# Performance work log

Hardware: AMD Instinct MI355X
Metric: run time of the kernel (lower is better)

The kernel has to match this reference:

```python
import jax, jax.numpy as jnp
import numpy as np

B, S, H, E = 4, 2048, 1024, 8

def setup_inputs() -> dict:
    key = jax.random.key(0)
    k1, k2, k3 = jax.random.split(key, 3)
    scale_g = 1.0 / np.sqrt(H)
    scale_e = 1.0 / np.sqrt(H)
    return {
        "x": jax.random.normal(k1, (B, S, H), dtype=jnp.float32),
        "gate_w": jax.random.normal(k2, (H, E), dtype=jnp.float32) * scale_g,
        "gate_b": jnp.zeros((E,), dtype=jnp.float32),
        "expert_w": jax.random.normal(k3, (E, H, H), dtype=jnp.float32) * scale_e,
        "expert_b": jnp.zeros((E, H), dtype=jnp.float32),
    }

def reference(x, gate_w, gate_b, expert_w, expert_b):
    b, s, h = x.shape
    tok = x.reshape(-1, h)                                  # [T, H]
    # gate: softmax over experts per token
    w = jax.nn.softmax(tok @ gate_w + gate_b, axis=-1)      # [T, E]
    # all experts applied to all tokens (dense MoE)
    eo = jnp.einsum("th,ehd->ted", tok, expert_w) + expert_b[None]  # [T, E, H]
    out = jnp.einsum("te,ted->td", w, eo)                   # [T, H]
    return out.reshape(b, s, h)
```

## Files before the change

### kernel.cpp

```cpp
#include <hip/hip_runtime.h>
#include <stdint.h>

typedef unsigned short u16;
typedef short bf8 __attribute__((ext_vector_type(8)));
typedef float f4 __attribute__((ext_vector_type(4)));

#define TTOK 8192
#define HD   1024
#define NE   8

static __device__ __forceinline__ u16 f2bf(float f) {
  union { float f; uint32_t u; } v; v.f = f;
  return (u16)((v.u + 0x7fffu + ((v.u >> 16) & 1u)) >> 16);
}

__global__ __launch_bounds__(256) void gate_conv_kernel(
    const float* __restrict__ x, const float* __restrict__ gw,
    const float* __restrict__ gb, float* __restrict__ wout,
    u16* __restrict__ abf)
{
  const int t    = blockIdx.x * 4 + (threadIdx.x >> 6);
  const int lane = threadIdx.x & 63;
  const float* xr = x + (size_t)t * HD;
  float p[NE];
#pragma unroll
  for (int e = 0; e < NE; ++e) p[e] = 0.f;
#pragma unroll 4
  for (int h = lane; h < HD; h += 64) {
    const float xv = xr[h];
    abf[(size_t)t * HD + h] = f2bf(xv);
    const float* g = gw + (size_t)h * NE;
#pragma unroll
    for (int e = 0; e < NE; ++e) p[e] += xv * g[e];
  }
#pragma unroll
  for (int e = 0; e < NE; ++e) {
#pragma unroll
    for (int off = 32; off > 0; off >>= 1)
      p[e] += __shfl_xor(p[e], off, 64);
    p[e] += gb[e];
  }
  float m = p[0];
#pragma unroll
  for (int e = 1; e < NE; ++e) m = fmaxf(m, p[e]);
  float s = 0.f;
#pragma unroll
  for (int e = 0; e < NE; ++e) { p[e] = expf(p[e] - m); s += p[e]; }
  const float inv = 1.f / s;
  if (lane == 0) {
#pragma unroll
    for (int e = 0; e < NE; ++e) wout[t * NE + e] = p[e] * inv;
  }
}

__global__ __launch_bounds__(256) void wconv_kernel(
    const float* __restrict__ ew, u16* __restrict__ wt)
{
  __shared__ u16 tile[64][66];
  const int e  = blockIdx.z;
  const int h0 = blockIdx.y * 64;
  const int d0 = blockIdx.x * 64;
  const int c  = threadIdx.x & 63;
  const int r0 = threadIdx.x >> 6;
  const float* src = ew + (size_t)e * HD * HD;
  u16* dst = wt + (size_t)e * HD * HD;
#pragma unroll
  for (int i = 0; i < 16; ++i) {
    const int r = i * 4 + r0;
    tile[r][c] = f2bf(src[(size_t)(h0 + r) * HD + d0 + c]);
  }
  __syncthreads();
#pragma unroll
  for (int i = 0; i < 16; ++i) {
    const int r = i * 4 + r0;
    dst[(size_t)(d0 + r) * HD + h0 + c] = tile[c][r];
  }
}

#define BM 128
#define BN 256
#define BK 64

#define MM(a_, b_, c_) __builtin_amdgcn_mfma_f32_16x16x32_bf16((a_), (b_), (c_), 0, 0, 0)

#define LDFA(off_, m_, kk_) (*(const bf8*)((const char*)As + (off_) + \
    (size_t)(wrb + (m_) * 16 + l15) * 128 + ((((kk_) * 4 + lhi) ^ (l15 & 7)) << 4)))
#define LDFB(off_, n_, kk_) (*(const bf8*)((const char*)Bs + (off_) + \
    (size_t)(wcb + (n_) * 16 + l15) * 128 + ((((kk_) * 4 + lhi) ^ (l15 & 7)) << 4)))

#define GL(srcp_, dstp_) __builtin_amdgcn_global_load_lds( \
    (const __attribute__((address_space(1))) void*)(srcp_), \
    (__attribute__((address_space(3))) void*)(dstp_), 16, 0, 0)

#define STAGE_PA(sq_)                                               \
  {                                                                 \
    const int se_ = (sq_) >> 4;                                     \
    const int sk_ = ((sq_) & 15) << 6;                              \
    const u16* as_ = aSrc0 + sk_;                                   \
    const u16* bs_ = bSrc0 + (size_t)se_ * (HD * HD) + sk_;         \
    char* ad_ = (char*)As + stA + tid * 16;                         \
    char* bd_ = (char*)Bs + stB + tid * 16;                         \
    GL(as_,         ad_);                                           \
    GL(as_ + 65536, ad_ + 8192);                                    \
    GL(bs_,         bd_);                                           \
  }
#define STAGE_PB(sq_)                                               \
  {                                                                 \
    const int se_ = (sq_) >> 4;                                     \
    const int sk_ = ((sq_) & 15) << 6;                              \
    const u16* bs_ = bSrc0 + (size_t)se_ * (HD * HD) + sk_;         \
    char* bd_ = (char*)Bs + stB + tid * 16;                         \
    GL(bs_ +  65536, bd_ +  8192);                                  \
    GL(bs_ + 131072, bd_ + 16384);                                  \
    GL(bs_ + 196608, bd_ + 24576);                                  \
  }

#define MFMA16                                            \
    acc[0][0] = MM(a0, b0, acc[0][0]);                    \
    acc[1][0] = MM(a1, b0, acc[1][0]);                    \
    acc[2][0] = MM(a2, b0, acc[2][0]);                    \
    acc[3][0] = MM(a3, b0, acc[3][0]);                    \
    acc[0][1] = MM(a0, b1, acc[0][1]);                    \
    acc[1][1] = MM(a1, b1, acc[1][1]);                    \
    acc[2][1] = MM(a2, b1, acc[2][1]);                    \
    acc[3][1] = MM(a3, b1, acc[3][1]);                    \
    acc[0][2] = MM(a0, b2, acc[0][2]);                    \
    acc[1][2] = MM(a1, b2, acc[1][2]);                    \
    acc[2][2] = MM(a2, b2, acc[2][2]);                    \
    acc[3][2] = MM(a3, b2, acc[3][2]);                    \
    acc[0][3] = MM(a0, b3, acc[0][3]);                    \
    acc[1][3] = MM(a1, b3, acc[1][3]);                    \
    acc[2][3] = MM(a2, b3, acc[2][3]);                    \
    acc[3][3] = MM(a3, b3, acc[3][3]);

#define READS(kk_)                                        \
    bf8 a0 = LDFA(curA, 0, kk_);                          \
    bf8 a1 = LDFA(curA, 1, kk_);                          \
    bf8 a2 = LDFA(curA, 2, kk_);                          \
    bf8 a3 = LDFA(curA, 3, kk_);                          \
    bf8 b0 = LDFB(curB, 0, kk_);                          \
    bf8 b1 = LDFB(curB, 1, kk_);                          \
    bf8 b2 = LDFB(curB, 2, kk_);                          \
    bf8 b3 = LDFB(curB, 3, kk_);

#define FOLD(e_)                                                      \
  {                                                                   \
    _Pragma("unroll")                                                 \
    for (int mi = 0; mi < 4; ++mi) {                                  \
      const int r_ = wrb + mi * 16 + lhi * 4;                         \
      const float w0 = wgs[(r_ + 0) * 9 + (e_)];                      \
      const float w1 = wgs[(r_ + 1) * 9 + (e_)];                      \
      const float w2 = wgs[(r_ + 2) * 9 + (e_)];                      \
      const float w3 = wgs[(r_ + 3) * 9 + (e_)];                      \
      _Pragma("unroll")                                               \
      for (int ni = 0; ni < 4; ++ni) {                                \
        accO[mi][ni][0] += w0 * acc[mi][ni][0];                       \
        accO[mi][ni][1] += w1 * acc[mi][ni][1];                       \
        accO[mi][ni][2] += w2 * acc[mi][ni][2];                       \
        accO[mi][ni][3] += w3 * acc[mi][ni][3];                       \
        acc[mi][ni] = fz;                                             \
      }                                                               \
    }                                                                 \
  }

#define ADVANCE                                          \
    curA += 16384; if (curA == 49152) curA = 0;          \
    curB += 32768; if (curB == 98304) curB = 0;          \
    stA  += 16384; if (stA  == 49152) stA  = 0;          \
    stB  += 32768; if (stB  == 98304) stB  = 0;

#define BAR       __builtin_amdgcn_s_barrier();
#define LGKM0     asm volatile("s_waitcnt lgkmcnt(0)" ::: "memory");
#define PRIO1     __builtin_amdgcn_s_setprio(1);
#define PRIO0     __builtin_amdgcn_s_setprio(0);

__global__ __launch_bounds__(512, 2) void moe_gemm_kernel(
    const u16* __restrict__ A,
    const u16* __restrict__ Wt,
    const float* __restrict__ wg,
    const float* __restrict__ eb,
    float* __restrict__ out)
{
  __shared__ u16 As[3 * BM * BK];
  __shared__ u16 Bs[3 * BN * BK];
  __shared__ float wgs[BM * 9];

  const int bid   = blockIdx.x;
  const int xcd   = bid & 7;
  const int local = bid >> 3;
  const int bm    = xcd * 8 + (local >> 2);
  const int bn    = local & 3;
  const int row0  = bm * BM;
  const int col0  = bn * BN;

  const int tid  = threadIdx.x;
  const int lane = tid & 63;
  const int wid  = tid >> 6;
  const int wr   = wid >> 2;
  const int wc   = wid & 3;
  const int l15  = lane & 15;
  const int lhi  = lane >> 4;
  const int wrb  = wr * 64;
  const int wcb  = wc * 64;

  const int row_in = tid >> 3;
  const int gsw    = (tid & 7) ^ ((tid >> 3) & 7);
  const u16* aSrc0 = A  + (size_t)(row0 + row_in) * HD + gsw * 8;
  const u16* bSrc0 = Wt + (size_t)(col0 + row_in) * HD + gsw * 8;

  {
    const int i0 = tid, i1 = tid + 512;
    const float v0 = wg[(size_t)row0 * NE + i0];
    const float v1 = wg[(size_t)row0 * NE + i1];
    wgs[(i0 >> 3) * 9 + (i0 & 7)] = v0;
    wgs[(i1 >> 3) * 9 + (i1 & 7)] = v1;
  }
  LGKM0

  const f4 fz = {0.f, 0.f, 0.f, 0.f};
  f4 acc[4][4], accO[4][4];
#pragma unroll
  for (int i = 0; i < 4; ++i)
#pragma unroll
    for (int j = 0; j < 4; ++j) { acc[i][j] = fz; accO[i][j] = fz; }

  int curA = 0, curB = 0;
  int stA = 32768, stB = 65536;

  {
    int svA = stA, svB = stB;
    stA = 0; stB = 0;       STAGE_PA(0) STAGE_PB(0)
    stA = 16384; stB = 32768; STAGE_PA(1) STAGE_PB(1)
    stA = svA; stB = svB;
  }
  asm volatile("s_waitcnt vmcnt(6)" ::: "memory");
  BAR

  for (int q = 0; q < 126; ++q) {
    {
      READS(0)
      STAGE_PA(q + 2)
      BAR LGKM0 PRIO1
      MFMA16
      PRIO0 BAR
    }
    {
      READS(1)
      STAGE_PB(q + 2)
      BAR LGKM0 PRIO1
      MFMA16
      PRIO0
      asm volatile("s_waitcnt vmcnt(6)" ::: "memory");
      BAR
    }
    ADVANCE
    if ((q & 15) == 15) FOLD(q >> 4)
  }
  {
    { READS(0) BAR LGKM0 PRIO1 MFMA16 PRIO0 BAR }
    { READS(1) BAR LGKM0 PRIO1 MFMA16 PRIO0
      asm volatile("s_waitcnt vmcnt(0)" ::: "memory");
      BAR }
    ADVANCE
  }
  {
    { READS(0) MFMA16 }
    { READS(1) MFMA16 }
  }
  FOLD(7)

  float ebv[4][8];
#pragma unroll
  for (int ni = 0; ni < 4; ++ni) {
    const int d = col0 + wcb + ni * 16 + l15;
#pragma unroll
    for (int e2 = 0; e2 < NE; ++e2) ebv[ni][e2] = eb[(size_t)e2 * HD + d];
  }
#pragma unroll
  for (int mi = 0; mi < 4; ++mi) {
    const int r_ = wrb + mi * 16 + lhi * 4;
#pragma unroll
    for (int j = 0; j < 4; ++j) {
      const int t = row0 + r_ + j;
      const float* wrow = &wgs[(r_ + j) * 9];
#pragma unroll
      for (int ni = 0; ni < 4; ++ni) {
        const float bias =
            wrow[0] * ebv[ni][0] + wrow[1] * ebv[ni][1] +
            wrow[2] * ebv[ni][2] + wrow[3] * ebv[ni][3] +
            wrow[4] * ebv[ni][4] + wrow[5] * ebv[ni][5] +
            wrow[6] * ebv[ni][6] + wrow[7] * ebv[ni][7];
        const int d = col0 + wcb + ni * 16 + l15;
        out[(size_t)t * HD + d] = accO[mi][ni][j] + bias;
      }
    }
  }
}

extern "C" void kernel_launch(void* const* d_in, const int* in_sizes, int n_in,
                              void* d_out, int out_size, void* d_ws, size_t ws_size,
                              hipStream_t stream) {
  const float* x  = (const float*)d_in[0];
  const float* gw = (const float*)d_in[1];
  const float* gb = (const float*)d_in[2];
  const float* ew = (const float*)d_in[3];
  const float* eb = (const float*)d_in[4];
  float* out = (float*)d_out;

  char* ws = (char*)d_ws;
  u16*   abf   = (u16*)ws;
  u16*   wt    = (u16*)(ws + (size_t)16 * 1024 * 1024);
  float* wgate = (float*)(ws + (size_t)32 * 1024 * 1024);

  gate_conv_kernel<<<dim3(TTOK / 4), dim3(256), 0, stream>>>(x, gw, gb, wgate, abf);
  wconv_kernel<<<dim3(16, 16, 8), dim3(256), 0, stream>>>(ew, wt);
  moe_gemm_kernel<<<dim3((TTOK / BM) * (HD / BN)), dim3(512), 0, stream>>>(abf, wt, wgate, eb, out);
}
```

Baseline: 156.4 us.

## Shrink GEMM tile to 128x128 with 4 waves and double buffering

Halves the output tile width and the block size to 256 threads (4 waves). It replaces the triple-buffered LDS pipeline, which waited with vmcnt(6), with a simpler double buffer that waits for all loads at the start of each iteration. The block-to-tile mapping is remapped and the gate-weight preload is vectorized. This doubles the grid and lowers LDS use per block, aiming for better occupancy and load balance. In exchange, A-tile reuse per loaded B element drops and load latency is less well hidden.

```diff
diff --git a/kernel.cpp b/kernel.cpp
--- a/kernel.cpp
+++ b/kernel.cpp
@@ -78,7 +78,7 @@
 }
 
 #define BM 128
-#define BN 256
+#define BN 128
 #define BK 64
 
 #define MM(a_, b_, c_) __builtin_amdgcn_mfma_f32_16x16x32_bf16((a_), (b_), (c_), 0, 0, 0)
@@ -92,27 +92,26 @@
     (const __attribute__((address_space(1))) void*)(srcp_), \
     (__attribute__((address_space(3))) void*)(dstp_), 16, 0, 0)
 
-#define STAGE_PA(sq_)                                               \
+#define STAGE_A(sq_)                                                \
   {                                                                 \
-    const int se_ = (sq_) >> 4;                                     \
     const int sk_ = ((sq_) & 15) << 6;                              \
     const u16* as_ = aSrc0 + sk_;                                   \
-    const u16* bs_ = bSrc0 + (size_t)se_ * (HD * HD) + sk_;         \
-    char* ad_ = (char*)As + stA + tid * 16;                         \
-    char* bd_ = (char*)Bs + stB + tid * 16;                         \
-    GL(as_,         ad_);                                           \
-    GL(as_ + 65536, ad_ + 8192);                                    \
-    GL(bs_,         bd_);                                           \
-  }
-#define STAGE_PB(sq_)                                               \
+    char* ad_ = (char*)As + stO + tid * 16;                         \
+    GL(as_,          ad_);                                          \
+    GL(as_ + 32768,  ad_ +  4096);                                  \
+    GL(as_ + 65536,  ad_ +  8192);                                  \
+    GL(as_ + 98304,  ad_ + 12288);                                  \
+  }
+#define STAGE_B(sq_)                                                \
   {                                                                 \
     const int se_ = (sq_) >> 4;                                     \
     const int sk_ = ((sq_) & 15) << 6;                              \
     const u16* bs_ = bSrc0 + (size_t)se_ * (HD * HD) + sk_;         \
-    char* bd_ = (char*)Bs + stB + tid * 16;                         \
-    GL(bs_ +  65536, bd_ +  8192);                                  \
-    GL(bs_ + 131072, bd_ + 16384);                                  \
-    GL(bs_ + 196608, bd_ + 24576);                                  \
+    char* bd_ = (char*)Bs + stO + tid * 16;                         \
+    GL(bs_,          bd_);                                          \
+    GL(bs_ + 32768,  bd_ +  4096);                                  \
+    GL(bs_ + 65536,  bd_ +  8192);                                  \
+    GL(bs_ + 98304,  bd_ + 12288);                                  \
   }
 
 #define MFMA16                                            \
@@ -134,14 +133,14 @@
     acc[3][3] = MM(a3, b3, acc[3][3]);
 
 #define READS(kk_)                                        \
-    bf8 a0 = LDFA(curA, 0, kk_);                          \
-    bf8 a1 = LDFA(curA, 1, kk_);                          \
-    bf8 a2 = LDFA(curA, 2, kk_);                          \
-    bf8 a3 = LDFA(curA, 3, kk_);                          \
-    bf8 b0 = LDFB(curB, 0, kk_);                          \
-    bf8 b1 = LDFB(curB, 1, kk_);                          \
-    bf8 b2 = LDFB(curB, 2, kk_);                          \
-    bf8 b3 = LDFB(curB, 3, kk_);
+    bf8 a0 = LDFA(curO, 0, kk_);                          \
+    bf8 a1 = LDFA(curO, 1, kk_);                          \
+    bf8 a2 = LDFA(curO, 2, kk_);                          \
+    bf8 a3 = LDFA(curO, 3, kk_);                          \
+    bf8 b0 = LDFB(curO, 0, kk_);                          \
+    bf8 b1 = LDFB(curO, 1, kk_);                          \
+    bf8 b2 = LDFB(curO, 2, kk_);                          \
+    bf8 b3 = LDFB(curO, 3, kk_);
 
 #define FOLD(e_)                                                      \
   {                                                                   \
@@ -163,57 +162,54 @@
     }                                                                 \
   }
 
-#define ADVANCE                                          \
-    curA += 16384; if (curA == 49152) curA = 0;          \
-    curB += 32768; if (curB == 98304) curB = 0;          \
-    stA  += 16384; if (stA  == 49152) stA  = 0;          \
-    stB  += 32768; if (stB  == 98304) stB  = 0;
-
 #define BAR       __builtin_amdgcn_s_barrier();
 #define LGKM0     asm volatile("s_waitcnt lgkmcnt(0)" ::: "memory");
+#define VM0       asm volatile("s_waitcnt vmcnt(0)" ::: "memory");
 #define PRIO1     __builtin_amdgcn_s_setprio(1);
 #define PRIO0     __builtin_amdgcn_s_setprio(0);
 
-__global__ __launch_bounds__(512, 2) void moe_gemm_kernel(
+__global__ __launch_bounds__(256, 2) void moe_gemm_kernel(
     const u16* __restrict__ A,
     const u16* __restrict__ Wt,
     const float* __restrict__ wg,
     const float* __restrict__ eb,
     float* __restrict__ out)
 {
-  __shared__ u16 As[3 * BM * BK];
-  __shared__ u16 Bs[3 * BN * BK];
+  __shared__ u16 As[2 * BM * BK];
+  __shared__ u16 Bs[2 * BN * BK];
   __shared__ float wgs[BM * 9];
 
   const int bid   = blockIdx.x;
   const int xcd   = bid & 7;
   const int local = bid >> 3;
-  const int bm    = xcd * 8 + (local >> 2);
-  const int bn    = local & 3;
+  const int bm    = xcd * 8 + (local & 7);
+  const int bn    = local >> 3;
   const int row0  = bm * BM;
   const int col0  = bn * BN;
 
   const int tid  = threadIdx.x;
   const int lane = tid & 63;
   const int wid  = tid >> 6;
-  const int wr   = wid >> 2;
-  const int wc   = wid & 3;
+  const int wr   = wid >> 1;
+  const int wc   = wid & 1;
   const int l15  = lane & 15;
   const int lhi  = lane >> 4;
   const int wrb  = wr * 64;
   const int wcb  = wc * 64;
 
   const int row_in = tid >> 3;
-  const int gsw    = (tid & 7) ^ ((tid >> 3) & 7);
+  const int gsw    = (tid & 7) ^ (row_in & 7);
   const u16* aSrc0 = A  + (size_t)(row0 + row_in) * HD + gsw * 8;
   const u16* bSrc0 = Wt + (size_t)(col0 + row_in) * HD + gsw * 8;
 
   {
-    const int i0 = tid, i1 = tid + 512;
-    const float v0 = wg[(size_t)row0 * NE + i0];
-    const float v1 = wg[(size_t)row0 * NE + i1];
-    wgs[(i0 >> 3) * 9 + (i0 & 7)] = v0;
-    wgs[(i1 >> 3) * 9 + (i1 & 7)] = v1;
+    const f4 v = *(const f4*)(wg + (size_t)row0 * NE + tid * 4);
+    const int i0 = tid * 4;
+#pragma unroll
+    for (int j = 0; j < 4; ++j) {
+      const int idx = i0 + j;
+      wgs[(idx >> 3) * 9 + (idx & 7)] = v[j];
+    }
   }
   LGKM0
 
@@ -224,49 +220,34 @@
 #pragma unroll
     for (int j = 0; j < 4; ++j) { acc[i][j] = fz; accO[i][j] = fz; }
 
-  int curA = 0, curB = 0;
-  int stA = 32768, stB = 65536;
-
-  {
-    int svA = stA, svB = stB;
-    stA = 0; stB = 0;       STAGE_PA(0) STAGE_PB(0)
-    stA = 16384; stB = 32768; STAGE_PA(1) STAGE_PB(1)
-    stA = svA; stB = svB;
-  }
-  asm volatile("s_waitcnt vmcnt(6)" ::: "memory");
-  BAR
-
-  for (int q = 0; q < 126; ++q) {
+  int curO = 0, stO = 16384;
+
+  { const int svO = stO; stO = 0; STAGE_A(0) STAGE_B(0) stO = svO; }
+
+  for (int q = 0; q < 127; ++q) {
+    VM0
+    BAR
     {
       READS(0)
-      STAGE_PA(q + 2)
+      STAGE_A(q + 1)
       BAR LGKM0 PRIO1
       MFMA16
       PRIO0 BAR
     }
     {
       READS(1)
-      STAGE_PB(q + 2)
+      STAGE_B(q + 1)
       BAR LGKM0 PRIO1
       MFMA16
       PRIO0
-      asm volatile("s_waitcnt vmcnt(6)" ::: "memory");
-      BAR
-    }
-    ADVANCE
+    }
+    { const int t_ = curO; curO = stO; stO = t_; }
     if ((q & 15) == 15) FOLD(q >> 4)
   }
-  {
-    { READS(0) BAR LGKM0 PRIO1 MFMA16 PRIO0 BAR }
-    { READS(1) BAR LGKM0 PRIO1 MFMA16 PRIO0
-      asm volatile("s_waitcnt vmcnt(0)" ::: "memory");
-      BAR }
-    ADVANCE
-  }
-  {
-    { READS(0) MFMA16 }
-    { READS(1) MFMA16 }
-  }
+  VM0
+  BAR
+  { READS(0) BAR LGKM0 PRIO1 MFMA16 PRIO0 BAR }
+  { READS(1) BAR LGKM0 PRIO1 MFMA16 PRIO0 }
   FOLD(7)
 
   float ebv[4][8];
@@ -314,5 +295,5 @@
 
   gate_conv_kernel<<<dim3(TTOK / 4), dim3(256), 0, stream>>>(x, gw, gb, wgate, abf);
   wconv_kernel<<<dim3(16, 16, 8), dim3(256), 0, stream>>>(ew, wt);
-  moe_gemm_kernel<<<dim3((TTOK / BM) * (HD / BN)), dim3(512), 0, stream>>>(abf, wt, wgate, eb, out);
-}
+  moe_gemm_kernel<<<dim3((TTOK / BM) * (HD / BN)), dim3(256), 0, stream>>>(abf, wt, wgate, eb, out);
+}
```

Result: slower. 164.4 us (+5.1%).
